# Kernel optimization log

Measured on AMD Instinct MI355X. Metric: run time of the kernel, lower is better.

Reference implementation:

```python
import jax, jax.numpy as jnp
import numpy as np
import math
from jax import lax

NUM_POS = 128        # random_choice in pos_neg_sampling
NUM_TOT = 256        # pos + (128 + negative_padding) always totals 256
POS_W = 10.0         # positive_weight in compute_loss


def _conv(x, w, b, pad):
    y = lax.conv_general_dilated(x, w, (1, 1), pad,
                                 dimension_numbers=('NCHW', 'OIHW', 'NCHW'))
    return y + b[None, :, None, None]


def make_anchor_box(img_h, img_w, gh, gw):
    # torch.range(0, W, W/(gw-1)) == inclusive linspace with gw points
    xs = jnp.linspace(0.0, float(img_w), gw)
    ys = jnp.linspace(0.0, float(img_h), gh)
    gx, gy = jnp.meshgrid(xs, ys, indexing='ij')          # (gw, gh) like torch.meshgrid
    xy = jnp.stack([gx.reshape(-1), gy.reshape(-1)], -1).reshape(gh, gw, 2)
    whs = []
    for area in (128 * 128, 256 * 256, 512 * 512):
        for wr, hr in ((1, 1), (2, 1), (1, 2)):
            u = math.sqrt(area / (wr * hr))
            whs.append((wr * u, hr * u))
    wh = jnp.asarray(whs, jnp.float32)                    # (9, 2)
    xy9 = jnp.broadcast_to(xy[:, :, None, :], (gh, gw, 9, 2))
    wh9 = jnp.broadcast_to(wh[None, None], (gh, gw, 9, 2))
    boxes = jnp.concatenate([xy9, xy9 + wh9], -1)         # x1,y1,x2,y2
    return boxes.reshape(-1, 4)


def pairwise_iou(t, a):
    # t: [T,4], a: [A,4], xyxy -> [T,A]
    lt = jnp.maximum(t[:, None, :2], a[None, :, :2])
    rb = jnp.minimum(t[:, None, 2:], a[None, :, 2:])
    wh = jnp.clip(rb - lt, 0.0)
    inter = wh[..., 0] * wh[..., 1]
    at = (t[:, 2] - t[:, 0]) * (t[:, 3] - t[:, 1])
    aa = (a[:, 2] - a[:, 0]) * (a[:, 3] - a[:, 1])
    return inter / (at[:, None] + aa[None, :] - inter)


def box_encode(anchor, bbox):
    awh = anchor[:, 2:] - anchor[:, :2]
    bwh = bbox[:, 2:] - bbox[:, :2]
    ac = anchor[:, :2] + awh / 2
    bc = bbox[:, :2] + bwh / 2
    dxy = (bc - ac) / awh
    dwh = jnp.log(bwh / awh)
    return jnp.concatenate([dxy, dwh], 1)


def rpn_forward(x, target, conv_w, conv_b, bbox_w, bbox_b, score_w, score_b,
                img_h, img_w):
    gh, gw = x.shape[-2], x.shape[-1]
    h = jax.nn.relu(_conv(x[None], conv_w, conv_b, 'SAME'))
    bbox = jax.nn.relu(_conv(h, bbox_w, bbox_b, 'VALID')).reshape(-1, 4)   # [A,4]
    score = jax.nn.relu(_conv(h, score_w, score_b, 'VALID')).reshape(-1, 2)  # [A,2]
    anchors = make_anchor_box(img_h, img_w, gh, gw)                        # [A,4]

    iou = pairwise_iou(target, anchors)                                    # [T,A]
    max_iou = iou.max(0)
    tgt_idx = jnp.argmax(iou, 0)

    # deterministic replacement for np.random.choice sampling (fixed shapes)
    pos_score = jnp.where(max_iou > 0.7, max_iou, -1.0)
    pos_vals, pos_idx = lax.top_k(pos_score, NUM_POS)
    pos_valid = pos_vals > 0.0
    n_pos = jnp.sum(pos_valid.astype(jnp.int32))

    neg_score = jnp.where(max_iou < 0.3, 1.0 - max_iou, -1.0)
    neg_vals, neg_idx = lax.top_k(neg_score, NUM_TOT)
    neg_valid = (neg_vals > 0.0) & (jnp.arange(NUM_TOT) < (NUM_TOT - n_pos))

    bbox_pred = bbox[pos_idx]                                              # [128,4]
    scores_sel = score[jnp.concatenate([pos_idx, neg_idx])]                # [384,2]
    valid = jnp.concatenate([pos_valid, neg_valid]).astype(jnp.float32)

    tgt_scores = jnp.concatenate([
        jnp.tile(jnp.asarray([[1.0, 0.0]], jnp.float32), (NUM_POS, 1)),
        jnp.tile(jnp.asarray([[0.0, 1.0]], jnp.float32), (NUM_TOT, 1))], 0)

    matched = target[tgt_idx[pos_idx]]
    treg = box_encode(anchors[pos_idx], matched)

    ce = -jnp.sum(tgt_scores * jax.nn.log_softmax(scores_sel, -1), -1)
    score_loss = jnp.sum(ce * valid) / jnp.maximum(jnp.sum(valid), 1.0)

    d = bbox_pred - treg
    sl1 = jnp.where(jnp.abs(d) < 1.0, 0.5 * d * d, jnp.abs(d) - 0.5)
    pm = pos_valid.astype(jnp.float32)[:, None]
    reg_loss = jnp.sum(sl1 * pm) / jnp.maximum(jnp.sum(pm) * 4.0, 1.0)

    return score_loss + POS_W * reg_loss


def setup_inputs():
    key = jax.random.key(0)
    ks = jax.random.split(key, 8)
    cin, gh, gw, nt = 512, 128, 128, 64
    x = jax.random.normal(ks[0], (cin, gh, gw), jnp.float32)
    cxy = jax.random.uniform(ks[1], (nt, 2), minval=300.0, maxval=1748.0)
    wh = jax.random.uniform(ks[2], (nt, 2), minval=64.0, maxval=512.0)
    target = jnp.concatenate([cxy - wh / 2, cxy + wh / 2], -1)
    conv_w = jax.random.normal(ks[3], (cin, cin, 3, 3), jnp.float32) * 0.02
    conv_b = jnp.zeros((cin,), jnp.float32)
    bbox_w = jax.random.normal(ks[4], (36, cin, 1, 1), jnp.float32) * 0.02
    bbox_b = jnp.zeros((36,), jnp.float32)
    score_w = jax.random.normal(ks[5], (18, cin, 1, 1), jnp.float32) * 0.02
    score_b = jnp.zeros((18,), jnp.float32)
    return {'x': x, 'target': target, 'conv_w': conv_w, 'conv_b': conv_b,
            'bbox_w': bbox_w, 'bbox_b': bbox_b, 'score_w': score_w,
            'score_b': score_b, 'img_h': 2048, 'img_w': 2048}


def reference(x, target, conv_w, conv_b, bbox_w, bbox_b, score_w, score_b,
              img_h, img_w):
    return rpn_forward(x, target, conv_w, conv_b, bbox_w, bbox_b,
                       score_w, score_b, img_h, img_w)
```

## Files before the change

kernel.cpp:

```cpp
#include <hip/hip_runtime.h>
#include <cstdint>
#include <cstddef>

typedef unsigned long long ull;
typedef __bf16 bf16x8 __attribute__((ext_vector_type(8)));
typedef float f32x4 __attribute__((ext_vector_type(4)));

#define NA     147456
#define NT     64
#define KDIM   4608
#define NTASK  1280
#define CAND_CAP 4096
#define KSPLIT 4
#define NIOUB  576
#define NTRB   2048
#define NPREP2 512
#define NIMCB  2880

#define OFF_WB2   0
#define OFF_P2    4718592
#define OFF_H4    16515072
#define OFF_XT    27000832
#define OFF_MIOU  60555264
#define OFF_CAND  61145088
#define OFF_CPB   62324736
#define OFF_CBZ   62327040
#define OFF_NPOS  62329344
#define OFF_POSA  62329348
#define OFF_TREG  62329860
#define OFF_TASKS 62331908
#define OFF_OUT   62337028

#define UANC 90.509667991878f
__device__ __constant__ float WKa[9] = {128.0f, 2.0f*UANC, UANC, 256.0f, 4.0f*UANC, 2.0f*UANC, 512.0f, 8.0f*UANC, 4.0f*UANC};
__device__ __constant__ float HKa[9] = {128.0f, UANC, 2.0f*UANC, 256.0f, 2.0f*UANC, 4.0f*UANC, 512.0f, 4.0f*UANC, 8.0f*UANC};

__device__ __forceinline__ float iou_one(float x1, float y1, float x2, float y2, float4 t) {
#pragma clang fp contract(off)
  float ltx = fmaxf(t.x, x1), lty = fmaxf(t.y, y1);
  float rbx = fminf(t.z, x2), rby = fminf(t.w, y2);
  float wx = fmaxf(rbx - ltx, 0.0f);
  float wy = fmaxf(rby - lty, 0.0f);
  float inter = wx * wy;
  float at = (t.z - t.x) * (t.w - t.y);
  float aa = (x2 - x1) * (y2 - y1);
  return inter / ((at + aa) - inter);
}

__device__ __forceinline__ unsigned short f2bf(float f) {
  unsigned int u = __float_as_uint(f);
  unsigned int r = (u + 0x7fffu + ((u >> 16) & 1u)) >> 16;
  return (unsigned short)r;
}

__global__ __launch_bounds__(256) void k_pi(const float* __restrict__ cw,
    unsigned short* __restrict__ Wb2, const float* __restrict__ x,
    float* __restrict__ xt,
    const float* __restrict__ tgt, const int* __restrict__ imw,
    const int* __restrict__ imh, float* __restrict__ miou,
    ull* __restrict__ cand, int* __restrict__ cpb, int* __restrict__ cbz) {
  __shared__ __align__(16) char smem[20480];
  int blk = blockIdx.x;
  int tid = threadIdx.x;
  if (blk >= NIOUB + NTRB) {
    float* row = (float*)smem;
    int m = blk - (NIOUB + NTRB);
    const float* src = cw + (size_t)m * KDIM;
    for (int f = tid; f < KDIM; f += 256) {
      int cin = f / 9;
      row[cin * 10 + (f - cin * 9)] = src[f];
    }
    __syncthreads();
    for (int kc = tid; kc < 576; kc += 256) {
      int r = kc >> 6, c8 = kc & 63;
      int base = c8 * 80 + r;
      unsigned short o[8];
      #pragma unroll
      for (int j = 0; j < 8; ++j) o[j] = f2bf(row[base + j * 10]);
      *(uint4*)(Wb2 + ((size_t)kc * 512 + m) * 8) = *(const uint4*)o;
    }
    return;
  }
  if (blk >= NIOUB) {
    float* tile = (float*)smem;
    int tb = blk - NIOUB;
    int pix0 = (tb & 255) * 64;
    int cin0 = (tb >> 8) * 64;
    int pr = tid & 15, cr = tid >> 4;
    #pragma unroll
    for (int i = 0; i < 4; ++i) {
      int cin = cr + i * 16;
      float4 v = *(const float4*)(x + (size_t)(cin0 + cin) * 16384 + pix0 + pr * 4);
      tile[cin * 65 + pr * 4 + 0] = v.x;
      tile[cin * 65 + pr * 4 + 1] = v.y;
      tile[cin * 65 + pr * 4 + 2] = v.z;
      tile[cin * 65 + pr * 4 + 3] = v.w;
    }
    __syncthreads();
    #pragma unroll
    for (int i = 0; i < 4; ++i) {
      int pix = cr + i * 16;
      float4 v = {tile[(pr * 4 + 0) * 65 + pix], tile[(pr * 4 + 1) * 65 + pix],
                  tile[(pr * 4 + 2) * 65 + pix], tile[(pr * 4 + 3) * 65 + pix]};
      *(float4*)(xt + (size_t)(pix0 + pix) * 512 + cin0 + pr * 4) = v;
    }
    return;
  }
  float4* ts = (float4*)smem;
  int* wz = (int*)(smem + 1024);
  int* wc = wz + 4;
  if (tid < NT) ts[tid] = ((const float4*)tgt)[tid];
  __syncthreads();
  int a = blk * 256 + tid;
  int k = a % 9;
  int pq = a / 9;
  int p = pq >> 7, q = pq & 127;
  float dx = (float)(*imw) / 127.0f;
  float dyl = (float)(*imh) / 127.0f;
  float x1 = (float)p * dx, y1 = (float)q * dyl;
  float x2 = x1 + WKa[k], y2 = y1 + HKa[k];
  float best = -1.0f;
  #pragma unroll 8
  for (int t = 0; t < NT; ++t) best = fmaxf(best, iou_one(x1, y1, x2, y2, ts[t]));
  miou[a] = best;
  int lane = tid & 63, w = tid >> 6;
  ull bz = __ballot(best == 0.0f);
  bool isc = best > 0.7f;
  ull bc = __ballot(isc);
  if (lane == 0) { wz[w] = (int)__popcll(bz); wc[w] = (int)__popcll(bc); }
  __syncthreads();
  if (tid == 0) {
    cbz[blk] = wz[0] + wz[1] + wz[2] + wz[3];
    cpb[blk] = wc[0] + wc[1] + wc[2] + wc[3];
  }
  if (isc) {
    int woff = 0;
    for (int i = 0; i < w; ++i) woff += wc[i];
    int rank = woff + (int)__popcll(bc & ((1ull << lane) - 1ull));
    cand[blk * 256 + rank] = ((ull)__float_as_uint(best) << 32) | (ull)(0xFFFFFFFFu - (unsigned)a);
  }
}

__global__ __launch_bounds__(256) void k_selA(const ull* __restrict__ cand,
    const int* __restrict__ cpb, int* __restrict__ nposp, int* __restrict__ posa) {
  __shared__ ull keys[CAND_CAP];
  __shared__ ull bnd[1024];
  __shared__ int hist[1024];
  __shared__ int cpbL[576];
  __shared__ int base576[577];
  __shared__ int wtot[4];
  __shared__ int selCnt, bndCnt, Tbin, mAbove;
  int tid = threadIdx.x;
  int lane = tid & 63;
  for (int i = tid; i < 576; i += 256) cpbL[i] = cpb[i];
  for (int i = tid; i < 1024; i += 256) hist[i] = 0;
  __syncthreads();
  int e0 = 0, e1 = 0, sA = 0, scanA = 0;
  if (tid < 192) {
    e0 = cpbL[3 * tid]; e1 = cpbL[3 * tid + 1]; int e2 = cpbL[3 * tid + 2];
    sA = e0 + e1 + e2;
    scanA = sA;
    for (int off = 1; off < 64; off <<= 1) {
      int v = __shfl_up(scanA, off);
      if (lane >= off) scanA += v;
    }
    if (lane == 63) wtot[tid >> 6] = scanA;
  }
  __syncthreads();
  if (tid < 192) {
    int w = tid >> 6;
    int woff = 0;
    for (int i = 0; i < w; ++i) woff += wtot[i];
    int excl = woff + scanA - sA;
    base576[3 * tid]     = excl;
    base576[3 * tid + 1] = excl + e0;
    base576[3 * tid + 2] = excl + e0 + e1;
    if (tid == 191) base576[576] = excl + sA;
  }
  __syncthreads();
  int cnt = base576[576]; if (cnt > CAND_CAP) cnt = CAND_CAP;
  for (int i = tid; i < CAND_CAP; i += 256) if (i >= cnt) keys[i] = 0ull;
  for (int rk = tid; rk < cnt; rk += 256) {
    int lo = 0, hi = 576;
    while (hi - lo > 1) { int mid = (lo + hi) >> 1; if (base576[mid] <= rk) lo = mid; else hi = mid; }
    keys[rk] = cand[lo * 256 + (rk - base576[lo])];
  }
  __syncthreads();
  if (cnt <= 128) {
    if (tid < cnt) posa[tid] = (int)(0xFFFFFFFFu - (unsigned)(keys[tid] & 0xFFFFFFFFull));
    if (tid == 0) *nposp = cnt;
    return;
  }
  for (int i = tid; i < cnt; i += 256) {
    unsigned ib = (unsigned)(keys[i] >> 32);
    atomicAdd(&hist[(ib - 0x3F333334u) >> 13], 1);
  }
  __syncthreads();
  if (tid < 64) {
    int s = 0;
    #pragma unroll
    for (int t = 0; t < 16; ++t) s += hist[tid * 16 + t];
    int S = s;
    #pragma unroll
    for (int off = 1; off < 64; off <<= 1) {
      int u = __shfl_down(S, off);
      if (tid + off < 64) S += u;
    }
    ull mask = __ballot(S >= 128);
    int g = 63 - __clzll(mask);
    int aboveS = __shfl(S, (g + 1 < 64) ? g + 1 : 63);
    if (g == 63) aboveS = 0;
    if (tid == 0) {
      int run = aboveS, T = g * 16 + 15;
      for (int b = g * 16 + 15; b >= g * 16; --b) {
        int h = hist[b];
        if (run + h >= 128) { T = b; break; }
        run += h;
      }
      Tbin = T; mAbove = run; selCnt = 0; bndCnt = 0;
    }
  }
  __syncthreads();
  int T = Tbin, m = mAbove;
  for (int i = tid; i < cnt; i += 256) {
    ull kk = keys[i];
    unsigned ib = (unsigned)(kk >> 32);
    int b = (int)((ib - 0x3F333334u) >> 13);
    if (b > T) {
      int r = atomicAdd(&selCnt, 1);
      posa[r] = (int)(0xFFFFFFFFu - (unsigned)(kk & 0xFFFFFFFFull));
    } else if (b == T) {
      int r = atomicAdd(&bndCnt, 1);
      if (r < 1024) bnd[r] = kk;
    }
  }
  __syncthreads();
  int B = bndCnt;
  int need = 128 - m;
  if (B <= 1024) {
    int n2 = 2; while (n2 < B) n2 <<= 1;
    for (int i = tid; i < n2; i += 256) if (i >= B) bnd[i] = 0ull;
    for (int size = 2; size <= n2; size <<= 1)
      for (int stride = size >> 1; stride > 0; stride >>= 1) {
        __syncthreads();
        for (int t = tid; t < n2 / 2; t += 256) {
          int i = 2 * t - (t & (stride - 1));
          int j = i + stride;
          ull a = bnd[i], b2 = bnd[j];
          bool desc = ((i & size) == 0);
          if (desc ? (a < b2) : (a > b2)) { bnd[i] = b2; bnd[j] = a; }
        }
      }
    __syncthreads();
    if (tid < need) posa[m + tid] = (int)(0xFFFFFFFFu - (unsigned)(bnd[tid] & 0xFFFFFFFFull));
  } else {
    for (int size = 2; size <= CAND_CAP; size <<= 1)
      for (int stride = size >> 1; stride > 0; stride >>= 1) {
        __syncthreads();
        for (int t = tid; t < CAND_CAP / 2; t += 256) {
          int i = 2 * t - (t & (stride - 1));
          int j = i + stride;
          ull a = keys[i], b2 = keys[j];
          bool desc = ((i & size) == 0);
          if (desc ? (a < b2) : (a > b2)) { keys[i] = b2; keys[j] = a; }
        }
      }
    __syncthreads();
    if (tid < 128) posa[tid] = (int)(0xFFFFFFFFu - (unsigned)(keys[tid] & 0xFFFFFFFFull));
  }
  if (tid == 0) *nposp = 128;
}

__global__ __launch_bounds__(256) void k_selB(const float* __restrict__ miou,
    const int* __restrict__ cbz, const float* __restrict__ tgt,
    const int* __restrict__ imw, const int* __restrict__ imh,
    const int* __restrict__ nposp, const int* __restrict__ posa,
    float* __restrict__ treg, int* __restrict__ tasks) {
  __shared__ int nzbase[145];
  __shared__ float4 ts[NT];
  __shared__ int posi[128];
  __shared__ int negA[256];
  __shared__ int wsum[4];
  int tid = threadIdx.x;
  int lane = tid & 63;
  if (tid < NT) ts[tid] = ((const float4*)tgt)[tid];
  int np = *nposp;
  if (tid < np) posi[tid] = posa[tid];
  int sB = 0, scanB = 0;
  if (tid < 144) {
    int4 cz4 = *(const int4*)(cbz + 4 * tid);
    sB = cz4.x + cz4.y + cz4.z + cz4.w;
    scanB = sB;
    for (int off = 1; off < 64; off <<= 1) {
      int v = __shfl_up(scanB, off);
      if (lane >= off) scanB += v;
    }
    bool last = (tid < 128) ? (lane == 63) : (tid == 143);
    if (last) wsum[tid >> 6] = scanB;
  }
  __syncthreads();
  if (tid < 144) {
    int w = tid >> 6;
    int woff = 0;
    for (int i = 0; i < w; ++i) woff += wsum[i];
    nzbase[tid] = woff + scanB - sB;
    if (tid == 143) nzbase[144] = woff + scanB;
  }
  __syncthreads();
  int w = tid >> 6;
  for (int j = 0; j < 144; ++j) {
    if (nzbase[j] >= 256) break;
    int a0 = j * 1024 + tid * 4;
    float4 m4 = *(const float4*)(miou + a0);
    int f0 = (m4.x == 0.0f), f1 = (m4.y == 0.0f), f2 = (m4.z == 0.0f), f3 = (m4.w == 0.0f);
    int tsum = f0 + f1 + f2 + f3;
    int scan = tsum;
    for (int off = 1; off < 64; off <<= 1) {
      int v = __shfl_up(scan, off);
      if (lane >= off) scan += v;
    }
    if (lane == 63) wsum[w] = scan;
    __syncthreads();
    int woff = nzbase[j];
    for (int i = 0; i < w; ++i) woff += wsum[i];
    int r = woff + scan - tsum;
    if (f0) { if (r < 256) negA[r] = a0;     r++; }
    if (f1) { if (r < 256) negA[r] = a0 + 1; r++; }
    if (f2) { if (r < 256) negA[r] = a0 + 2; r++; }
    if (f3) { if (r < 256) negA[r] = a0 + 3;      }
    __syncthreads();
  }
  __syncthreads();
  if (tid < np) {
    int a = posi[tid];
    int k = a % 9; int pq = a / 9; int p = pq >> 7, q = pq & 127;
    float dx = (float)(*imw) / 127.0f, dyl = (float)(*imh) / 127.0f;
    float x1 = (float)p * dx, y1 = (float)q * dyl;
    float x2 = x1 + WKa[k], y2 = y1 + HKa[k];
    float best = -1.0f; int bt = 0;
    for (int t = 0; t < NT; ++t) {
      float v = iou_one(x1, y1, x2, y2, ts[t]);
      if (v > best) { best = v; bt = t; }
    }
    float4 m = ts[bt];
    float aw = x2 - x1, ah = y2 - y1;
    float acx = x1 + aw * 0.5f, acy = y1 + ah * 0.5f;
    float bwd = m.z - m.x, bhd = m.w - m.y;
    float bcx = m.x + bwd * 0.5f, bcy = m.y + bhd * 0.5f;
    treg[tid * 4 + 0] = (bcx - acx) / aw;
    treg[tid * 4 + 1] = (bcy - acy) / ah;
    treg[tid * 4 + 2] = logf(bwd / aw);
    treg[tid * 4 + 3] = logf(bhd / ah);
  }
  for (int t = tid; t < NTASK; t += 256) {
    int rec = 0;
    if (t < 768) {
      int s = t / 6, jj = t - s * 6;
      if (s < np) {
        int a = posi[s];
        int f, wr, xx;
        if (jj < 4) { f = 4 * a; wr = f >> 14; xx = (f & 127) + jj; }
        else        { f = 2 * a; wr = 36 + (f >> 14); xx = (f & 127) + (jj - 4); }
        int yy = (f >> 7) & 127;
        rec = (int)(0x80000000u | ((unsigned)wr << 16) | ((unsigned)yy << 8) | (unsigned)xx);
      }
    } else {
      int s = (t - 768) >> 1, jj = (t - 768) & 1;
      if (s < 256 - np) {
        int a = negA[s];
        int f = 2 * a; int wr = 36 + (f >> 14); int yy = (f >> 7) & 127; int xx = (f & 127) + jj;
        rec = (int)(0x80000000u | ((unsigned)wr << 16) | ((unsigned)yy << 8) | (unsigned)xx);
      }
    }
    tasks[t] = rec;
  }
}

__global__ __launch_bounds__(256) void k_im2col(const float* __restrict__ xt,
    const int* __restrict__ tasks, unsigned short* __restrict__ P2) {
  int idx = blockIdx.x * 256 + threadIdx.x;
  int t = idx / 576;
  int kc = idx - t * 576;
  int r = kc >> 6, c8 = kc & 63;
  int rec = tasks[t];
  unsigned short o[8];
  bool valid = false;
  int pix = 0;
  if (rec < 0) {
    int py = (rec >> 8) & 127, px = rec & 127;
    int dy = r / 3;
    int yy = py + dy - 1, xx = px + (r - dy * 3) - 1;
    if (yy >= 0 && yy < 128 && xx >= 0 && xx < 128) { valid = true; pix = yy * 128 + xx; }
  }
  if (valid) {
    const float4* src = (const float4*)(xt + (size_t)pix * 512 + c8 * 8);
    float4 v0 = src[0], v1 = src[1];
    o[0] = f2bf(v0.x); o[1] = f2bf(v0.y); o[2] = f2bf(v0.z); o[3] = f2bf(v0.w);
    o[4] = f2bf(v1.x); o[5] = f2bf(v1.y); o[6] = f2bf(v1.z); o[7] = f2bf(v1.w);
  } else {
    #pragma unroll
    for (int j = 0; j < 8; ++j) o[j] = 0;
  }
  *(uint4*)(P2 + ((size_t)kc * NTASK + t) * 8) = *(const uint4*)o;
}

__global__ __launch_bounds__(256) void k_mfma(const unsigned short* __restrict__ Wb2,
    const unsigned short* __restrict__ P2, const int* __restrict__ nposp,
    float* __restrict__ H4) {
  int npos = *nposp;
  int tt0 = blockIdx.x * 128;
  int posend = 6 * npos, negend = 768 + 2 * (256 - npos);
  if (!((tt0 < posend) || ((tt0 + 128 > 768) && (tt0 < negend)))) return;
  int c0 = blockIdx.y * 128;
  int ks = blockIdx.z;
  int tid = threadIdx.x;
  int wave = tid >> 6, lane = tid & 63;
  int quad = lane >> 4, r = lane & 15;
  int m_base = c0 + (wave & 1) * 64;
  int n_base = tt0 + (wave >> 1) * 64;
  int kc0 = ks * 144 + quad;
  const bf16x8* Ab = (const bf16x8*)Wb2 + ((size_t)kc0 * 512 + m_base + r);
  const bf16x8* Bb = (const bf16x8*)P2 + ((size_t)kc0 * NTASK + n_base + r);

  f32x4 acc[4][4];
  #pragma unroll
  for (int i = 0; i < 4; ++i)
    #pragma unroll
    for (int j = 0; j < 4; ++j) acc[i][j] = (f32x4){0.f, 0.f, 0.f, 0.f};

  bf16x8 a[4], b[4];
  #pragma unroll
  for (int mi = 0; mi < 4; ++mi) a[mi] = Ab[mi * 16];
  #pragma unroll
  for (int ni = 0; ni < 4; ++ni) b[ni] = Bb[ni * 16];

  for (int s = 0; s < 36; ++s) {
    bf16x8 an[4], bn[4];
    if (s < 35) {
      const bf16x8* An = Ab + (size_t)(s + 1) * 4 * 512;
      const bf16x8* Bn = Bb + (size_t)(s + 1) * 4 * NTASK;
      #pragma unroll
      for (int mi = 0; mi < 4; ++mi) an[mi] = An[mi * 16];
      #pragma unroll
      for (int ni = 0; ni < 4; ++ni) bn[ni] = Bn[ni * 16];
    }
    #pragma unroll
    for (int mi = 0; mi < 4; ++mi)
      #pragma unroll
      for (int ni = 0; ni < 4; ++ni)
        acc[mi][ni] = __builtin_amdgcn_mfma_f32_16x16x32_bf16(a[mi], b[ni], acc[mi][ni], 0, 0, 0);
    if (s < 35) {
      #pragma unroll
      for (int mi = 0; mi < 4; ++mi) a[mi] = an[mi];
      #pragma unroll
      for (int ni = 0; ni < 4; ++ni) b[ni] = bn[ni];
    }
  }
  size_t hb = (size_t)ks * NTASK;
  #pragma unroll
  for (int mi = 0; mi < 4; ++mi) {
    int c = m_base + mi * 16 + quad * 4;
    #pragma unroll
    for (int ni = 0; ni < 4; ++ni) {
      int t = n_base + ni * 16 + r;
      *(f32x4*)(H4 + (hb + t) * 512 + c) = acc[mi][ni];
    }
  }
}

__global__ __launch_bounds__(256) void k_out(const float* __restrict__ H4,
    const int* __restrict__ tasks,
    const float* __restrict__ cb, const float* __restrict__ bw,
    const float* __restrict__ bb, const float* __restrict__ sw,
    const float* __restrict__ sb, float* __restrict__ outv) {
  int wave = threadIdx.x >> 6, lane = threadIdx.x & 63;
  int t = blockIdx.x * 4 + wave;
  int rec = tasks[t];
  if (rec >= 0) return;
  int wr = (rec >> 16) & 63;
  const float* wrow = (wr < 36) ? (bw + wr * 512) : (sw + (wr - 36) * 512);
  float s = 0.0f;
  #pragma unroll
  for (int it = 0; it < 8; ++it) {
    int c = it * 64 + lane;
    size_t o = (size_t)t * 512 + c;
    float hv = H4[o] + H4[o + 1280 * 512] + H4[o + 2 * 1280 * 512] + H4[o + 3 * 1280 * 512] + cb[c];
    s = fmaf(fmaxf(hv, 0.0f), wrow[c], s);
  }
  #pragma unroll
  for (int off = 32; off > 0; off >>= 1) s += __shfl_down(s, off);
  if (lane == 0) {
    float b = (wr < 36) ? bb[wr] : sb[wr - 36];
    outv[t] = fmaxf(s + b, 0.0f);
  }
}

__global__ __launch_bounds__(256) void k_loss(const float* __restrict__ outv,
    const float* __restrict__ treg, const int* __restrict__ nposp,
    float* __restrict__ out) {
  __shared__ float r1[256], r2[256];
  int tid = threadIdx.x;
  int np = *nposp;
  float ce = 0.0f;
  for (int r = tid; r < 384; r += 256) {
    bool valid = (r < 128) ? (r < np) : ((r - 128) < 256 - np);
    if (valid) {
      int t0 = (r < 128) ? (r * 6 + 4) : (768 + 2 * (r - 128));
      float s0 = outv[t0], s1 = outv[t0 + 1];
      float mm = fmaxf(s0, s1);
      float lse = mm + logf(expf(s0 - mm) + expf(s1 - mm));
      ce += lse - ((r < 128) ? s0 : s1);
    }
  }
  float rg = 0.0f;
  for (int r = tid; r < 512; r += 256) {
    if ((r >> 2) < np) {
      float d = outv[(r >> 2) * 6 + (r & 3)] - treg[r];
      float ad = fabsf(d);
      rg += (ad < 1.0f) ? 0.5f * d * d : ad - 0.5f;
    }
  }
  r1[tid] = ce; r2[tid] = rg;
  __syncthreads();
  for (int s = 128; s > 0; s >>= 1) {
    if (tid < s) { r1[tid] += r1[tid + s]; r2[tid] += r2[tid + s]; }
    __syncthreads();
  }
  if (tid == 0) {
    float score_loss = r1[0] / 256.0f;
    float reg_loss = r2[0] / fmaxf(4.0f * (float)np, 1.0f);
    out[0] = score_loss + 10.0f * reg_loss;
  }
}

extern "C" void kernel_launch(void* const* d_in, const int* in_sizes, int n_in,
                              void* d_out, int out_size, void* d_ws, size_t ws_size,
                              hipStream_t stream) {
  const float* x   = (const float*)d_in[0];
  const float* tgt = (const float*)d_in[1];
  const float* cw  = (const float*)d_in[2];
  const float* cb  = (const float*)d_in[3];
  const float* bw  = (const float*)d_in[4];
  const float* bb  = (const float*)d_in[5];
  const float* sw  = (const float*)d_in[6];
  const float* sb  = (const float*)d_in[7];
  const int* imh   = (const int*)d_in[8];
  const int* imw   = (const int*)d_in[9];

  char* ws = (char*)d_ws;
  unsigned short* Wb2 = (unsigned short*)(ws + OFF_WB2);
  unsigned short* P2  = (unsigned short*)(ws + OFF_P2);
  float* H4    = (float*)(ws + OFF_H4);
  float* xt    = (float*)(ws + OFF_XT);
  float* miou  = (float*)(ws + OFF_MIOU);
  ull*   cand  = (ull*)(ws + OFF_CAND);
  int*   cpb   = (int*)(ws + OFF_CPB);
  int*   cbz   = (int*)(ws + OFF_CBZ);
  int*   nposp = (int*)(ws + OFF_NPOS);
  int*   posa  = (int*)(ws + OFF_POSA);
  float* treg  = (float*)(ws + OFF_TREG);
  int*   tasks = (int*)(ws + OFF_TASKS);
  float* outv  = (float*)(ws + OFF_OUT);
  float* out   = (float*)d_out;

  k_pi    <<<dim3(NIOUB + NTRB + NPREP2), dim3(256), 0, stream>>>(cw, Wb2, x, xt, tgt, imw, imh, miou, cand, cpb, cbz);
  k_selA  <<<dim3(1),             dim3(256), 0, stream>>>(cand, cpb, nposp, posa);
  k_selB  <<<dim3(1),             dim3(256), 0, stream>>>(miou, cbz, tgt, imw, imh, nposp, posa, treg, tasks);
  k_im2col<<<dim3(NIMCB),         dim3(256), 0, stream>>>(xt, tasks, P2);
  k_mfma  <<<dim3(10, 4, KSPLIT), dim3(256), 0, stream>>>(Wb2, P2, nposp, H4);
  k_out   <<<dim3(320),           dim3(256), 0, stream>>>(H4, tasks, cb, bw, bb, sw, sb, outv);
  k_loss  <<<dim3(1),             dim3(256), 0, stream>>>(outv, treg, nposp, out);
}
```

Before: 167.3 us.

## Drop full input transpose; gather im2col directly from x for selected anchors

Removes the full 32MB NCHW→NHWC transpose of x and instead gathers the 3x3 neighbourhoods of only the selected positions directly from x into shared memory, then emits the bf16 im2col rows per run of adjacent tasks. Merges the two single-block selection kernels into one, which also emits the run descriptors. Retiles the MFMA GEMM to 64x64 tiles with the K-split moved across waves within a block. The cost removed is the large transpose traffic and one launch. The gather reads strided columns from NCHW, which may be poorly coalesced.

```diff
diff --git a/kernel.cpp b/kernel.cpp
--- a/kernel.cpp
+++ b/kernel.cpp
@@ -11,25 +11,21 @@
 #define KDIM   4608
 #define NTASK  1280
 #define CAND_CAP 4096
-#define KSPLIT 4
 #define NIOUB  576
-#define NTRB   2048
-#define NPREP2 512
-#define NIMCB  2880
+#define NPREPB 512
 
 #define OFF_WB2   0
 #define OFF_P2    4718592
 #define OFF_H4    16515072
-#define OFF_XT    27000832
-#define OFF_MIOU  60555264
-#define OFF_CAND  61145088
-#define OFF_CPB   62324736
-#define OFF_CBZ   62327040
-#define OFF_NPOS  62329344
-#define OFF_POSA  62329348
-#define OFF_TREG  62329860
-#define OFF_TASKS 62331908
-#define OFF_OUT   62337028
+#define OFF_MIOU  27000832
+#define OFF_CAND  27590656
+#define OFF_CPB   28770304
+#define OFF_CBZ   28772608
+#define OFF_NPOS  28774912
+#define OFF_TREG  28774920
+#define OFF_TASKS 28776968
+#define OFF_RUNS  28782088
+#define OFF_OUT   28784136
 
 #define UANC 90.509667991878f
 __device__ __constant__ float WKa[9] = {128.0f, 2.0f*UANC, UANC, 256.0f, 4.0f*UANC, 2.0f*UANC, 512.0f, 8.0f*UANC, 4.0f*UANC};
@@ -54,17 +50,16 @@
 }
 
 __global__ __launch_bounds__(256) void k_pi(const float* __restrict__ cw,
-    unsigned short* __restrict__ Wb2, const float* __restrict__ x,
-    float* __restrict__ xt,
+    unsigned short* __restrict__ Wb2,
     const float* __restrict__ tgt, const int* __restrict__ imw,
     const int* __restrict__ imh, float* __restrict__ miou,
     ull* __restrict__ cand, int* __restrict__ cpb, int* __restrict__ cbz) {
   __shared__ __align__(16) char smem[20480];
   int blk = blockIdx.x;
   int tid = threadIdx.x;
-  if (blk >= NIOUB + NTRB) {
+  if (blk >= NIOUB) {
     float* row = (float*)smem;
-    int m = blk - (NIOUB + NTRB);
+    int m = blk - NIOUB;
     const float* src = cw + (size_t)m * KDIM;
     for (int f = tid; f < KDIM; f += 256) {
       int cin = f / 9;
@@ -78,31 +73,6 @@
       #pragma unroll
       for (int j = 0; j < 8; ++j) o[j] = f2bf(row[base + j * 10]);
       *(uint4*)(Wb2 + ((size_t)kc * 512 + m) * 8) = *(const uint4*)o;
-    }
-    return;
-  }
-  if (blk >= NIOUB) {
-    float* tile = (float*)smem;
-    int tb = blk - NIOUB;
-    int pix0 = (tb & 255) * 64;
-    int cin0 = (tb >> 8) * 64;
-    int pr = tid & 15, cr = tid >> 4;
-    #pragma unroll
-    for (int i = 0; i < 4; ++i) {
-      int cin = cr + i * 16;
-      float4 v = *(const float4*)(x + (size_t)(cin0 + cin) * 16384 + pix0 + pr * 4);
-      tile[cin * 65 + pr * 4 + 0] = v.x;
-      tile[cin * 65 + pr * 4 + 1] = v.y;
-      tile[cin * 65 + pr * 4 + 2] = v.z;
-      tile[cin * 65 + pr * 4 + 3] = v.w;
-    }
-    __syncthreads();
-    #pragma unroll
-    for (int i = 0; i < 4; ++i) {
-      int pix = cr + i * 16;
-      float4 v = {tile[(pr * 4 + 0) * 65 + pix], tile[(pr * 4 + 1) * 65 + pix],
-                  tile[(pr * 4 + 2) * 65 + pix], tile[(pr * 4 + 3) * 65 + pix]};
-      *(float4*)(xt + (size_t)(pix0 + pix) * 512 + cin0 + pr * 4) = v;
     }
     return;
   }
@@ -141,17 +111,27 @@
   }
 }
 
-__global__ __launch_bounds__(256) void k_selA(const ull* __restrict__ cand,
-    const int* __restrict__ cpb, int* __restrict__ nposp, int* __restrict__ posa) {
+__global__ __launch_bounds__(256) void k_sel(const float* __restrict__ miou,
+    const ull* __restrict__ cand, const int* __restrict__ cpb,
+    const int* __restrict__ cbz, const float* __restrict__ tgt,
+    const int* __restrict__ imw, const int* __restrict__ imh,
+    int* __restrict__ nposp, float* __restrict__ treg, int* __restrict__ tasks,
+    int* __restrict__ runs) {
   __shared__ ull keys[CAND_CAP];
   __shared__ ull bnd[1024];
   __shared__ int hist[1024];
   __shared__ int cpbL[576];
   __shared__ int base576[577];
+  __shared__ int nzbase[145];
+  __shared__ float4 ts[NT];
+  __shared__ int posi[128];
+  __shared__ int negA[256];
   __shared__ int wtot[4];
+  __shared__ int wsum[4];
   __shared__ int selCnt, bndCnt, Tbin, mAbove;
   int tid = threadIdx.x;
   int lane = tid & 63;
+  if (tid < NT) ts[tid] = ((const float4*)tgt)[tid];
   for (int i = tid; i < 576; i += 256) cpbL[i] = cpb[i];
   for (int i = tid; i < 1024; i += 256) hist[i] = 0;
   __syncthreads();
@@ -165,6 +145,18 @@
       if (lane >= off) scanA += v;
     }
     if (lane == 63) wtot[tid >> 6] = scanA;
+  }
+  int sB = 0, scanB = 0;
+  if (tid < 144) {
+    int4 cz4 = *(const int4*)(cbz + 4 * tid);
+    sB = cz4.x + cz4.y + cz4.z + cz4.w;
+    scanB = sB;
+    for (int off = 1; off < 64; off <<= 1) {
+      int v = __shfl_up(scanB, off);
+      if (lane >= off) scanB += v;
+    }
+    bool last = (tid < 128) ? (lane == 63) : (tid == 143);
+    if (last) wsum[tid >> 6] = scanB;
   }
   __syncthreads();
   if (tid < 192) {
@@ -177,6 +169,13 @@
     base576[3 * tid + 2] = excl + e0 + e1;
     if (tid == 191) base576[576] = excl + sA;
   }
+  if (tid < 144) {
+    int w = tid >> 6;
+    int woff = 0;
+    for (int i = 0; i < w; ++i) woff += wsum[i];
+    nzbase[tid] = woff + scanB - sB;
+    if (tid == 143) nzbase[144] = woff + scanB;
+  }
   __syncthreads();
   int cnt = base576[576]; if (cnt > CAND_CAP) cnt = CAND_CAP;
   for (int i = tid; i < CAND_CAP; i += 256) if (i >= cnt) keys[i] = 0ull;
@@ -186,126 +185,91 @@
     keys[rk] = cand[lo * 256 + (rk - base576[lo])];
   }
   __syncthreads();
+  int np;
   if (cnt <= 128) {
-    if (tid < cnt) posa[tid] = (int)(0xFFFFFFFFu - (unsigned)(keys[tid] & 0xFFFFFFFFull));
-    if (tid == 0) *nposp = cnt;
-    return;
-  }
-  for (int i = tid; i < cnt; i += 256) {
-    unsigned ib = (unsigned)(keys[i] >> 32);
-    atomicAdd(&hist[(ib - 0x3F333334u) >> 13], 1);
-  }
-  __syncthreads();
-  if (tid < 64) {
-    int s = 0;
-    #pragma unroll
-    for (int t = 0; t < 16; ++t) s += hist[tid * 16 + t];
-    int S = s;
-    #pragma unroll
-    for (int off = 1; off < 64; off <<= 1) {
-      int u = __shfl_down(S, off);
-      if (tid + off < 64) S += u;
-    }
-    ull mask = __ballot(S >= 128);
-    int g = 63 - __clzll(mask);
-    int aboveS = __shfl(S, (g + 1 < 64) ? g + 1 : 63);
-    if (g == 63) aboveS = 0;
-    if (tid == 0) {
-      int run = aboveS, T = g * 16 + 15;
-      for (int b = g * 16 + 15; b >= g * 16; --b) {
-        int h = hist[b];
-        if (run + h >= 128) { T = b; break; }
-        run += h;
-      }
-      Tbin = T; mAbove = run; selCnt = 0; bndCnt = 0;
-    }
-  }
-  __syncthreads();
-  int T = Tbin, m = mAbove;
-  for (int i = tid; i < cnt; i += 256) {
-    ull kk = keys[i];
-    unsigned ib = (unsigned)(kk >> 32);
-    int b = (int)((ib - 0x3F333334u) >> 13);
-    if (b > T) {
-      int r = atomicAdd(&selCnt, 1);
-      posa[r] = (int)(0xFFFFFFFFu - (unsigned)(kk & 0xFFFFFFFFull));
-    } else if (b == T) {
-      int r = atomicAdd(&bndCnt, 1);
-      if (r < 1024) bnd[r] = kk;
-    }
-  }
-  __syncthreads();
-  int B = bndCnt;
-  int need = 128 - m;
-  if (B <= 1024) {
-    int n2 = 2; while (n2 < B) n2 <<= 1;
-    for (int i = tid; i < n2; i += 256) if (i >= B) bnd[i] = 0ull;
-    for (int size = 2; size <= n2; size <<= 1)
-      for (int stride = size >> 1; stride > 0; stride >>= 1) {
-        __syncthreads();
-        for (int t = tid; t < n2 / 2; t += 256) {
-          int i = 2 * t - (t & (stride - 1));
-          int j = i + stride;
-          ull a = bnd[i], b2 = bnd[j];
-          bool desc = ((i & size) == 0);
-          if (desc ? (a < b2) : (a > b2)) { bnd[i] = b2; bnd[j] = a; }
+    np = cnt;
+    if (tid < cnt) posi[tid] = (int)(0xFFFFFFFFu - (unsigned)(keys[tid] & 0xFFFFFFFFull));
+  } else {
+    np = 128;
+    for (int i = tid; i < cnt; i += 256) {
+      unsigned ib = (unsigned)(keys[i] >> 32);
+      atomicAdd(&hist[(ib - 0x3F333334u) >> 13], 1);
+    }
+    __syncthreads();
+    if (tid < 64) {
+      int s = 0;
+      #pragma unroll
+      for (int t = 0; t < 16; ++t) s += hist[tid * 16 + t];
+      int S = s;
+      #pragma unroll
+      for (int off = 1; off < 64; off <<= 1) {
+        int u = __shfl_down(S, off);
+        if (tid + off < 64) S += u;
+      }
+      ull mask = __ballot(S >= 128);
+      int g = 63 - __clzll(mask);
+      int aboveS = __shfl(S, (g + 1 < 64) ? g + 1 : 63);
+      if (g == 63) aboveS = 0;
+      if (tid == 0) {
+        int run = aboveS, T = g * 16 + 15;
+        for (int b = g * 16 + 15; b >= g * 16; --b) {
+          int h = hist[b];
+          if (run + h >= 128) { T = b; break; }
+          run += h;
         }
-      }
-    __syncthreads();
-    if (tid < need) posa[m + tid] = (int)(0xFFFFFFFFu - (unsigned)(bnd[tid] & 0xFFFFFFFFull));
-  } else {
-    for (int size = 2; size <= CAND_CAP; size <<= 1)
-      for (int stride = size >> 1; stride > 0; stride >>= 1) {
-        __syncthreads();
-        for (int t = tid; t < CAND_CAP / 2; t += 256) {
-          int i = 2 * t - (t & (stride - 1));
-          int j = i + stride;
-          ull a = keys[i], b2 = keys[j];
-          bool desc = ((i & size) == 0);
-          if (desc ? (a < b2) : (a > b2)) { keys[i] = b2; keys[j] = a; }
+        Tbin = T; mAbove = run; selCnt = 0; bndCnt = 0;
+      }
+    }
+    __syncthreads();
+    int T = Tbin, m = mAbove;
+    for (int i = tid; i < cnt; i += 256) {
+      ull kk = keys[i];
+      unsigned ib = (unsigned)(kk >> 32);
+      int b = (int)((ib - 0x3F333334u) >> 13);
+      if (b > T) {
+        int r = atomicAdd(&selCnt, 1);
+        posi[r] = (int)(0xFFFFFFFFu - (unsigned)(kk & 0xFFFFFFFFull));
+      } else if (b == T) {
+        int r = atomicAdd(&bndCnt, 1);
+        if (r < 1024) bnd[r] = kk;
+      }
+    }
+    __syncthreads();
+    int B = bndCnt;
+    int need = 128 - m;
+    if (B <= 1024) {
+      int n2 = 2; while (n2 < B) n2 <<= 1;
+      for (int i = tid; i < n2; i += 256) if (i >= B) bnd[i] = 0ull;
+      for (int size = 2; size <= n2; size <<= 1)
+        for (int stride = size >> 1; stride > 0; stride >>= 1) {
+          __syncthreads();
+          for (int t = tid; t < n2 / 2; t += 256) {
+            int i = 2 * t - (t & (stride - 1));
+            int j = i + stride;
+            ull a = bnd[i], b2 = bnd[j];
+            bool desc = ((i & size) == 0);
+            if (desc ? (a < b2) : (a > b2)) { bnd[i] = b2; bnd[j] = a; }
+          }
         }
-      }
-    __syncthreads();
-    if (tid < 128) posa[tid] = (int)(0xFFFFFFFFu - (unsigned)(keys[tid] & 0xFFFFFFFFull));
-  }
-  if (tid == 0) *nposp = 128;
-}
-
-__global__ __launch_bounds__(256) void k_selB(const float* __restrict__ miou,
-    const int* __restrict__ cbz, const float* __restrict__ tgt,
-    const int* __restrict__ imw, const int* __restrict__ imh,
-    const int* __restrict__ nposp, const int* __restrict__ posa,
-    float* __restrict__ treg, int* __restrict__ tasks) {
-  __shared__ int nzbase[145];
-  __shared__ float4 ts[NT];
-  __shared__ int posi[128];
-  __shared__ int negA[256];
-  __shared__ int wsum[4];
-  int tid = threadIdx.x;
-  int lane = tid & 63;
-  if (tid < NT) ts[tid] = ((const float4*)tgt)[tid];
-  int np = *nposp;
-  if (tid < np) posi[tid] = posa[tid];
-  int sB = 0, scanB = 0;
-  if (tid < 144) {
-    int4 cz4 = *(const int4*)(cbz + 4 * tid);
-    sB = cz4.x + cz4.y + cz4.z + cz4.w;
-    scanB = sB;
-    for (int off = 1; off < 64; off <<= 1) {
-      int v = __shfl_up(scanB, off);
-      if (lane >= off) scanB += v;
-    }
-    bool last = (tid < 128) ? (lane == 63) : (tid == 143);
-    if (last) wsum[tid >> 6] = scanB;
-  }
-  __syncthreads();
-  if (tid < 144) {
-    int w = tid >> 6;
-    int woff = 0;
-    for (int i = 0; i < w; ++i) woff += wsum[i];
-    nzbase[tid] = woff + scanB - sB;
-    if (tid == 143) nzbase[144] = woff + scanB;
-  }
+      __syncthreads();
+      if (tid < need) posi[m + tid] = (int)(0xFFFFFFFFu - (unsigned)(bnd[tid] & 0xFFFFFFFFull));
+    } else {
+      for (int size = 2; size <= CAND_CAP; size <<= 1)
+        for (int stride = size >> 1; stride > 0; stride >>= 1) {
+          __syncthreads();
+          for (int t = tid; t < CAND_CAP / 2; t += 256) {
+            int i = 2 * t - (t & (stride - 1));
+            int j = i + stride;
+            ull a = keys[i], b2 = keys[j];
+            bool desc = ((i & size) == 0);
+            if (desc ? (a < b2) : (a > b2)) { keys[i] = b2; keys[j] = a; }
+          }
+        }
+      __syncthreads();
+      if (tid < 128) posi[tid] = (int)(0xFFFFFFFFu - (unsigned)(keys[tid] & 0xFFFFFFFFull));
+    }
+  }
+  if (tid == 0) *nposp = np;
   __syncthreads();
   int w = tid >> 6;
   for (int j = 0; j < 144; ++j) {
@@ -374,53 +338,101 @@
     }
     tasks[t] = rec;
   }
-}
-
-__global__ __launch_bounds__(256) void k_im2col(const float* __restrict__ xt,
-    const int* __restrict__ tasks, unsigned short* __restrict__ P2) {
-  int idx = blockIdx.x * 256 + threadIdx.x;
-  int t = idx / 576;
-  int kc = idx - t * 576;
-  int r = kc >> 6, c8 = kc & 63;
-  int rec = tasks[t];
-  unsigned short o[8];
-  bool valid = false;
-  int pix = 0;
-  if (rec < 0) {
-    int py = (rec >> 8) & 127, px = rec & 127;
-    int dy = r / 3;
-    int yy = py + dy - 1, xx = px + (r - dy * 3) - 1;
-    if (yy >= 0 && yy < 128 && xx >= 0 && xx < 128) { valid = true; pix = yy * 128 + xx; }
-  }
-  if (valid) {
-    const float4* src = (const float4*)(xt + (size_t)pix * 512 + c8 * 8);
-    float4 v0 = src[0], v1 = src[1];
-    o[0] = f2bf(v0.x); o[1] = f2bf(v0.y); o[2] = f2bf(v0.z); o[3] = f2bf(v0.w);
-    o[4] = f2bf(v1.x); o[5] = f2bf(v1.y); o[6] = f2bf(v1.z); o[7] = f2bf(v1.w);
-  } else {
+  for (int s2 = tid; s2 < 512; s2 += 256) {
+    int rec;
+    if (s2 < 256) {
+      int s = s2 >> 1;
+      int odd = s2 & 1;
+      int tb = 6 * s + (odd ? 4 : 0);
+      int wide = odd ? 0 : (1 << 25);
+      if (s < np) {
+        int a = posi[s];
+        int f = odd ? 2 * a : 4 * a;
+        rec = (int)(0x80000000u | (unsigned)wide | ((unsigned)tb << 14) |
+                    ((unsigned)((f >> 7) & 127) << 7) | (unsigned)(f & 127));
+      } else {
+        rec = wide | (tb << 14);
+      }
+    } else {
+      int s = s2 - 256;
+      int tb = 768 + 2 * s;
+      if (s < 256 - np) {
+        int a = negA[s];
+        int f = 2 * a;
+        rec = (int)(0x80000000u | ((unsigned)tb << 14) |
+                    ((unsigned)((f >> 7) & 127) << 7) | (unsigned)(f & 127));
+      } else {
+        rec = tb << 14;
+      }
+    }
+    runs[s2] = rec;
+  }
+}
+
+__global__ __launch_bounds__(256) void k_gather(const float* __restrict__ x,
+    const int* __restrict__ runs, unsigned short* __restrict__ P2) {
+  __shared__ __align__(16) unsigned short L[3 * 6 * 520];
+  int tid = threadIdx.x;
+  int rec = runs[blockIdx.x];
+  int wide = (rec >> 25) & 1;
+  int ntasks = wide ? 4 : 2;
+  int tb = (rec >> 14) & 2047;
+  int total = 576 * ntasks;
+  if (rec >= 0) {
+    uint4 z = {0, 0, 0, 0};
+    for (int w = tid; w < total; w += 256) {
+      int kc, lt;
+      if (wide) { kc = w >> 2; lt = w & 3; } else { kc = w >> 1; lt = w & 1; }
+      *(uint4*)(P2 + ((size_t)kc * NTASK + tb + lt) * 8) = z;
+    }
+    return;
+  }
+  int py = (rec >> 7) & 127, px = rec & 127;
+  #pragma unroll
+  for (int i = 0; i < 3; ++i) {
+    int pair = i * 256 + tid;
+    int cin = (pair & 255) * 2;
+    int dy = pair >> 8;
+    int row = py + dy - 1;
+    bool rowok = (row >= 0) && (row < 128);
+    const float* s0 = x + (size_t)cin * 16384 + row * 128;
+    const float* s1 = s0 + 16384;
     #pragma unroll
-    for (int j = 0; j < 8; ++j) o[j] = 0;
-  }
-  *(uint4*)(P2 + ((size_t)kc * NTASK + t) * 8) = *(const uint4*)o;
+    for (int c = 0; c < 6; ++c) {
+      int xx = px - 1 + c;
+      bool ok = rowok && (xx >= 0) && (xx < 128);
+      float v0 = ok ? s0[xx] : 0.0f;
+      float v1 = ok ? s1[xx] : 0.0f;
+      unsigned pk = ((unsigned)f2bf(v1) << 16) | (unsigned)f2bf(v0);
+      *(unsigned*)&L[(dy * 6 + c) * 520 + cin] = pk;
+    }
+  }
+  __syncthreads();
+  for (int w = tid; w < total; w += 256) {
+    int kc, lt;
+    if (wide) { kc = w >> 2; lt = w & 3; } else { kc = w >> 1; lt = w & 1; }
+    int r = kc >> 6, c8 = kc & 63;
+    int dy = r / 3, dxp = r - dy * 3;
+    int col = lt + dxp;
+    uint4 frag = *(const uint4*)&L[(dy * 6 + col) * 520 + c8 * 8];
+    *(uint4*)(P2 + ((size_t)kc * NTASK + tb + lt) * 8) = frag;
+  }
 }
 
 __global__ __launch_bounds__(256) void k_mfma(const unsigned short* __restrict__ Wb2,
     const unsigned short* __restrict__ P2, const int* __restrict__ nposp,
     float* __restrict__ H4) {
   int npos = *nposp;
-  int tt0 = blockIdx.x * 128;
+  int tt0 = blockIdx.x * 64;
   int posend = 6 * npos, negend = 768 + 2 * (256 - npos);
-  if (!((tt0 < posend) || ((tt0 + 128 > 768) && (tt0 < negend)))) return;
-  int c0 = blockIdx.y * 128;
-  int ks = blockIdx.z;
+  if (!((tt0 < posend) || ((tt0 + 64 > 768) && (tt0 < negend)))) return;
+  int c0 = blockIdx.y * 64;
   int tid = threadIdx.x;
   int wave = tid >> 6, lane = tid & 63;
   int quad = lane >> 4, r = lane & 15;
-  int m_base = c0 + (wave & 1) * 64;
-  int n_base = tt0 + (wave >> 1) * 64;
-  int kc0 = ks * 144 + quad;
-  const bf16x8* Ab = (const bf16x8*)Wb2 + ((size_t)kc0 * 512 + m_base + r);
-  const bf16x8* Bb = (const bf16x8*)P2 + ((size_t)kc0 * NTASK + n_base + r);
+  int kc0 = wave * 144 + quad;
+  const bf16x8* Ab = (const bf16x8*)Wb2 + ((size_t)kc0 * 512 + c0 + r);
+  const bf16x8* Bb = (const bf16x8*)P2 + ((size_t)kc0 * NTASK + tt0 + r);
 
   f32x4 acc[4][4];
   #pragma unroll
@@ -456,13 +468,13 @@
       for (int ni = 0; ni < 4; ++ni) b[ni] = bn[ni];
     }
   }
-  size_t hb = (size_t)ks * NTASK;
+  size_t hb = (size_t)wave * NTASK;
   #pragma unroll
   for (int mi = 0; mi < 4; ++mi) {
-    int c = m_base + mi * 16 + quad * 4;
+    int c = c0 + mi * 16 + quad * 4;
     #pragma unroll
     for (int ni = 0; ni < 4; ++ni) {
-      int t = n_base + ni * 16 + r;
+      int t = tt0 + ni * 16 + r;
       *(f32x4*)(H4 + (hb + t) * 512 + c) = acc[mi][ni];
     }
   }
@@ -551,23 +563,21 @@
   unsigned short* Wb2 = (unsigned short*)(ws + OFF_WB2);
   unsigned short* P2  = (unsigned short*)(ws + OFF_P2);
   float* H4    = (float*)(ws + OFF_H4);
-  float* xt    = (float*)(ws + OFF_XT);
   float* miou  = (float*)(ws + OFF_MIOU);
   ull*   cand  = (ull*)(ws + OFF_CAND);
   int*   cpb   = (int*)(ws + OFF_CPB);
   int*   cbz   = (int*)(ws + OFF_CBZ);
   int*   nposp = (int*)(ws + OFF_NPOS);
-  int*   posa  = (int*)(ws + OFF_POSA);
   float* treg  = (float*)(ws + OFF_TREG);
   int*   tasks = (int*)(ws + OFF_TASKS);
+  int*   runs  = (int*)(ws + OFF_RUNS);
   float* outv  = (float*)(ws + OFF_OUT);
   float* out   = (float*)d_out;
 
-  k_pi    <<<dim3(NIOUB + NTRB + NPREP2), dim3(256), 0, stream>>>(cw, Wb2, x, xt, tgt, imw, imh, miou, cand, cpb, cbz);
-  k_selA  <<<dim3(1),             dim3(256), 0, stream>>>(cand, cpb, nposp, posa);
-  k_selB  <<<dim3(1),             dim3(256), 0, stream>>>(miou, cbz, tgt, imw, imh, nposp, posa, treg, tasks);
-  k_im2col<<<dim3(NIMCB),         dim3(256), 0, stream>>>(xt, tasks, P2);
-  k_mfma  <<<dim3(10, 4, KSPLIT), dim3(256), 0, stream>>>(Wb2, P2, nposp, H4);
-  k_out   <<<dim3(320),           dim3(256), 0, stream>>>(H4, tasks, cb, bw, bb, sw, sb, outv);
-  k_loss  <<<dim3(1),             dim3(256), 0, stream>>>(outv, treg, nposp, out);
-}
+  k_pi    <<<dim3(NIOUB + NPREPB), dim3(256), 0, stream>>>(cw, Wb2, tgt, imw, imh, miou, cand, cpb, cbz);
+  k_sel   <<<dim3(1),              dim3(256), 0, stream>>>(miou, cand, cpb, cbz, tgt, imw, imh, nposp, treg, tasks, runs);
+  k_gather<<<dim3(512),            dim3(256), 0, stream>>>(x, runs, P2);
+  k_mfma  <<<dim3(20, 8),          dim3(256), 0, stream>>>(Wb2, P2, nposp, H4);
+  k_out   <<<dim3(320),            dim3(256), 0, stream>>>(H4, tasks, cb, bw, bb, sw, sb, outv);
+  k_loss  <<<dim3(1),              dim3(256), 0, stream>>>(outv, treg, nposp, out);
+}
```

Result: slower. 179.9 us (+7.5%).
